# Kernel optimization log

Measured on AMD Instinct MI355X. Metric: run time of the kernel, lower is better.

The kernel has to match this reference:

```python
import jax, jax.numpy as jnp
import numpy as np

NH, NP, MA, FL = 8, 4, 2, 3   # heads, points, max_num_agent, feature_level
L = MA * FL                    # total sampling levels = 6
C = 256
BS, NQ = 8, 4096
SS = np.array([[64, 64], [32, 32], [16, 16]] * MA, dtype=np.int64)  # [L,2] (H,W)
NV = int((SS[:, 0] * SS[:, 1]).sum())  # 10752


def setup_inputs() -> dict:
    key = jax.random.key(0)
    ks = jax.random.split(key, 8)
    f32 = jnp.float32
    return {
        'query': jax.random.normal(ks[0], (BS, NQ, C), f32),
        'query_pos': jax.random.normal(ks[1], (BS, NQ, C), f32),
        'value': jax.random.normal(ks[2], (BS, NV, C), f32),
        'reference_points': jax.random.uniform(ks[3], (BS, NQ, L, 2), f32),
        'spatial_shapes': SS,
        'W_off': jax.random.normal(ks[4], (C, L * NH * NP * 2), f32) * 0.01,
        'b_off': jnp.zeros((L * NH * NP * 2,), f32),
        'W_attn': jax.random.normal(ks[5], (C, L * NH * NP), f32) * 0.05,
        'b_attn': jnp.zeros((L * NH * NP,), f32),
        'W_val': jax.random.normal(ks[6], (C, C), f32) * 0.05,
        'b_val': jnp.zeros((C,), f32),
        'W_out': jax.random.normal(ks[7], (C, C), f32) * 0.05,
        'b_out': jnp.zeros((C,), f32),
    }


def _ms_deform_attn(v, loc, attn, ss):
    # v: [bs, nv, NH, d]; loc: [bs, nq, NH, L, NP, 2] in [0,1] (x,y)
    # attn: [bs, nq, NH, L, NP]; ss: np int array [L,2] (H,W) -- static
    bs, nq = loc.shape[0], loc.shape[1]
    d = v.shape[-1]
    starts = np.concatenate([[0], np.cumsum(ss[:, 0] * ss[:, 1])[:-1]])
    out = jnp.zeros((bs, NH, nq, d), v.dtype)
    for l in range(L):
        H, W = int(ss[l, 0]), int(ss[l, 1])
        s0 = int(starts[l])
        vl = v[:, s0:s0 + H * W].transpose(0, 2, 1, 3)  # [bs, NH, HW, d]
        # sampling coords, grid_sample align_corners=False convention
        x = loc[:, :, :, l, :, 0].transpose(0, 2, 1, 3) * W - 0.5  # [bs,NH,nq,NP]
        y = loc[:, :, :, l, :, 1].transpose(0, 2, 1, 3) * H - 0.5
        x0 = jnp.floor(x); y0 = jnp.floor(y)
        lx = x - x0; ly = y - y0
        x0i = x0.astype(jnp.int32); y0i = y0.astype(jnp.int32)

        def gather(yi, xi):
            valid = (yi >= 0) & (yi < H) & (xi >= 0) & (xi < W)
            idx = jnp.clip(yi, 0, H - 1) * W + jnp.clip(xi, 0, W - 1)  # [bs,NH,nq,NP]
            g = jnp.take_along_axis(vl, idx.reshape(bs, NH, nq * NP, 1), axis=2)
            g = g.reshape(bs, NH, nq, NP, d)
            return g * valid[..., None].astype(g.dtype)  # zero padding outside

        sampled = ((1 - lx) * (1 - ly))[..., None] * gather(y0i, x0i) \
                + (lx * (1 - ly))[..., None] * gather(y0i, x0i + 1) \
                + ((1 - lx) * ly)[..., None] * gather(y0i + 1, x0i) \
                + (lx * ly)[..., None] * gather(y0i + 1, x0i + 1)
        aw = attn[:, :, :, l, :].transpose(0, 2, 1, 3)  # [bs,NH,nq,NP]
        out = out + jnp.einsum('bhqpd,bhqp->bhqd', sampled, aw)
    return out.transpose(0, 2, 1, 3).reshape(bs, nq, NH * d)


def reference(query, query_pos, value, reference_points, spatial_shapes,
              W_off, b_off, W_attn, b_attn, W_val, b_val, W_out, b_out):
    ss = np.asarray(spatial_shapes)
    identity = query
    q = query + query_pos
    bs, nv, c = value.shape
    nq = q.shape[1]
    v = (value @ W_val + b_val).reshape(bs, nv, NH, c // NH)
    off = (q @ W_off + b_off).reshape(bs, nq, NH, L, NP, 2)
    attn = (q @ W_attn + b_attn).reshape(bs, nq, NH, L * NP)
    attn = jax.nn.softmax(attn, axis=-1).reshape(bs, nq, NH, L, NP)
    offset_normalizer = jnp.asarray(np.stack([ss[:, 1], ss[:, 0]], -1), q.dtype)  # [L,2] (W,H)
    loc = reference_points[:, :, None, :, None, :] \
        + off / offset_normalizer[None, None, None, :, None, :]
    out = _ms_deform_attn(v, loc, attn, ss)
    out = out @ W_out + b_out
    return out + identity  # dropout is identity in eval mode
```

## Files before the change

### kernel.cpp

```cpp
#include <hip/hip_runtime.h>

#define NHEAD 8
#define NPOINT 4
#define NLVL 6
#define CDIM 256
#define BSZ 8
#define NQRY 4096
#define NVAL 10752

typedef __attribute__((ext_vector_type(8))) short short8;
typedef __attribute__((ext_vector_type(4))) float floatx4;
typedef __attribute__((ext_vector_type(2))) float float2v;

__device__ __forceinline__ unsigned short f2bf(float f) {
    unsigned u = __float_as_uint(f);
    return (unsigned short)((u + 0x7FFFu + ((u >> 16) & 1u)) >> 16);
}
__device__ __forceinline__ unsigned pack2(float a, float b) {
    return (unsigned)f2bf(a) | ((unsigned)f2bf(b) << 16);
}
__device__ __forceinline__ float blo(unsigned u) { return __uint_as_float(u << 16); }
__device__ __forceinline__ float bhi(unsigned u) { return __uint_as_float(u & 0xffff0000u); }

__device__ __forceinline__ void gload16(const void* g, void* l) {
    __builtin_amdgcn_global_load_lds(
        (const __attribute__((address_space(1))) unsigned int*)g,
        (__attribute__((address_space(3))) unsigned int*)l, 16, 0, 0);
}

__global__ __launch_bounds__(256) void prep_w(
    const float* __restrict__ Wv, const float* __restrict__ Woff,
    const float* __restrict__ Wattn, const float* __restrict__ Wo,
    unsigned short* __restrict__ Wt)
{
    const int id = blockIdx.x * 256 + threadIdx.x;
    const int n = id >> 8, k = id & 255;
    float val;
    if (n < 256) val = Wv[k * 256 + n];
    else if (n < 832) {
        const int nn = n - 256;
        val = (nn < 384) ? Woff[k * 384 + nn] : Wattn[k * 192 + (nn - 384)];
    } else val = Wo[k * 256 + (n - 832)];
    Wt[id] = f2bf(val);
}

__global__ __launch_bounds__(256) void q_conv(
    const float* __restrict__ query, const float* __restrict__ qpos,
    unsigned short* __restrict__ qbf)
{
    const long i = ((long)blockIdx.x * 256 + threadIdx.x) * 4;
    const float4 a = *(const float4*)(query + i);
    const float4 b = *(const float4*)(qpos + i);
    ushort4 r;
    r.x = f2bf(a.x + b.x); r.y = f2bf(a.y + b.y);
    r.z = f2bf(a.z + b.z); r.w = f2bf(a.w + b.w);
    *(ushort4*)(qbf + i) = r;
}

template<int BN, int ABF, int VTRANS, int RESID, int SPLITB>
__global__ __launch_bounds__(512) void gemm_mfma(
    const void* __restrict__ Av, const unsigned short* __restrict__ Bt,
    const float* __restrict__ bias, const float* __restrict__ bias2,
    const float* __restrict__ resid, void* __restrict__ Cv,
    int M, int Ntot)
{
    constexpr int BK = 64, BMt = 128;
    constexpr int WN = BN / 4, NT = WN / 16;
    constexpr int ACH = BMt * (BK / 8);
    constexpr int BCH = BN * (BK / 8);
    constexpr int NCH = ACH + BCH;
    __shared__ char smem[NCH * 16];
    const int tid = threadIdx.x;
    const int bm = blockIdx.y * BMt;
    const int bcol = blockIdx.x * BN;
    const int wid = tid >> 6, lane = tid & 63;
    const int wm = (wid >> 2) * 64, wn = (wid & 3) * WN;
    const int lm = lane & 15;

    floatx4 acc[4][NT];
#pragma unroll
    for (int i = 0; i < 4; ++i)
#pragma unroll
        for (int j = 0; j < NT; ++j) acc[i][j] = (floatx4)0.0f;

    for (int k0 = 0; k0 < 256; k0 += BK) {
        if (ABF) {
            const unsigned short* A = (const unsigned short*)Av;
            constexpr int NI = NCH / 512;
#pragma unroll
            for (int j = 0; j < NI; ++j) {
                const int cbase = (wid * NI + j) * 64;
                const int g = cbase + lane;
                const unsigned short* src;
                if (cbase < ACH) {
                    const int row = g >> 3, c = (g & 7) ^ (row & 7);
                    src = A + (long)(bm + row) * 256 + k0 + c * 8;
                } else {
                    const int g2 = g - ACH;
                    const int row = g2 >> 3, c = (g2 & 7) ^ (row & 7);
                    src = Bt + (long)(bcol + row) * 256 + k0 + c * 8;
                }
                gload16(src, smem + cbase * 16);
            }
        } else {
            constexpr int NIB = BCH / 512;
#pragma unroll
            for (int j = 0; j < NIB; ++j) {
                const int cbase = (wid * NIB + j) * 64;
                const int g2 = cbase + lane;
                const int row = g2 >> 3, c = (g2 & 7) ^ (row & 7);
                gload16(Bt + (long)(bcol + row) * 256 + k0 + c * 8,
                        smem + ACH * 16 + cbase * 16);
            }
            const float* A = (const float*)Av;
#pragma unroll
            for (int j = 0; j < 2; ++j) {
                const int g = j * 512 + tid;
                const int row = g >> 3, c = g & 7;
                const float* p = A + (long)(bm + row) * 256 + k0 + c * 8;
                const float4 a = *(const float4*)p;
                const float4 b = *(const float4*)(p + 4);
                uint4 v;
                v.x = pack2(a.x, a.y); v.y = pack2(a.z, a.w);
                v.z = pack2(b.x, b.y); v.w = pack2(b.z, b.w);
                *(uint4*)(smem + row * 128 + ((c ^ (row & 7)) << 4)) = v;
            }
        }
        __syncthreads();

#pragma unroll
        for (int kk = 0; kk < 2; ++kk) {
            const int cc = kk * 4 + (lane >> 4);
            short8 af[4], bfr[NT];
#pragma unroll
            for (int i = 0; i < 4; ++i) {
                const int row = wm + i * 16 + lm;
                af[i] = *(const short8*)(smem + row * 128 + ((cc ^ (row & 7)) << 4));
            }
#pragma unroll
            for (int j = 0; j < NT; ++j) {
                const int row = wn + j * 16 + lm;
                bfr[j] = *(const short8*)(smem + ACH * 16 + row * 128 + ((cc ^ (row & 7)) << 4));
            }
#pragma unroll
            for (int i = 0; i < 4; ++i)
#pragma unroll
                for (int j = 0; j < NT; ++j)
                    acc[i][j] = __builtin_amdgcn_mfma_f32_16x16x32_bf16(bfr[j], af[i], acc[i][j], 0, 0, 0);
        }
        __syncthreads();
    }

    const int qrow = (lane >> 4) * 4;
#pragma unroll
    for (int j = 0; j < NT; ++j) {
        const int colg = bcol + wn + j * 16 + qrow;
        float4 bv4;
        if (SPLITB && colg >= 384) bv4 = *(const float4*)(bias2 + colg - 384);
        else                       bv4 = *(const float4*)(bias + colg);
#pragma unroll
        for (int i = 0; i < 4; ++i) {
            const int rowl = wm + i * 16 + lm;
            const int rowg = bm + rowl;
            float v0 = acc[i][j][0] + bv4.x;
            float v1 = acc[i][j][1] + bv4.y;
            float v2 = acc[i][j][2] + bv4.z;
            float v3 = acc[i][j][3] + bv4.w;
            if (VTRANS) {
                const int b = bm / NVAL;
                const int pos = bm - b * NVAL + rowl;
                const int h = colg >> 5, d = colg & 31;
                ushort4 o;
                o.x = f2bf(v0); o.y = f2bf(v1); o.z = f2bf(v2); o.w = f2bf(v3);
                *(ushort4*)&((unsigned short*)Cv)[
                    (((long)(b * NHEAD + h)) * NVAL + pos) * 32 + d] = o;
            } else {
                if (RESID) {
                    const float4 rr = *(const float4*)(resid + (long)rowg * 256 + colg);
                    v0 += rr.x; v1 += rr.y; v2 += rr.z; v3 += rr.w;
                }
                float4 o; o.x = v0; o.y = v1; o.z = v2; o.w = v3;
                *(float4*)&((float*)Cv)[(long)rowg * Ntot + colg] = o;
            }
        }
    }
}

__global__ __launch_bounds__(256) void ms_sample4(
    const unsigned short* __restrict__ v,
    const float* __restrict__ oa,
    const float* __restrict__ refp,
    unsigned short* __restrict__ outi)
{
    __shared__ float s_rec[4][192 * 6];
    __shared__ float s_ref[4][12];
    const int tid = threadIdx.x;
    const int w = tid >> 6;
    const int lane = tid & 63;
    const int bq = blockIdx.x * 4 + w;
    const int b = bq >> 12;

    if (lane < 12) s_ref[w][lane] = refp[(long)bq * 12 + lane];
    __syncthreads();

    const int h = lane >> 3;
    const int li = lane & 7;
    const float* oarow = oa + (long)bq * 576;

    const float* lgp = oarow + 384 + h * 24 + li * 3;
    const float lg0 = lgp[0], lg1 = lgp[1], lg2 = lgp[2];
    float mx = fmaxf(lg0, fmaxf(lg1, lg2));
    mx = fmaxf(mx, __shfl_xor(mx, 1));
    mx = fmaxf(mx, __shfl_xor(mx, 2));
    mx = fmaxf(mx, __shfl_xor(mx, 4));
    const float e0 = __expf(lg0 - mx);
    const float e1 = __expf(lg1 - mx);
    const float e2 = __expf(lg2 - mx);
    float den = e0 + e1 + e2;
    den += __shfl_xor(den, 1);
    den += __shfl_xor(den, 2);
    den += __shfl_xor(den, 4);
    const float inv = 1.0f / den;
    const float aw_[3] = {e0 * inv, e1 * inv, e2 * inv};

    const float* offp = oarow + (h * 24 + li * 3) * 2;
    const float2v od0 = *(const float2v*)(offp);
    const float2v od1 = *(const float2v*)(offp + 2);
    const float2v od2 = *(const float2v*)(offp + 4);

#pragma unroll
    for (int k = 0; k < 3; ++k) {
        const int lp = li * 3 + k;
        const int l = lp >> 2;
        const int sh = (l >= 3) ? (l - 3) : l;
        const int W = 64 >> sh;
        const int base = ((l >= 3) ? 5376 : 0)
                       + ((sh >= 1) ? 4096 : 0)
                       + ((sh >= 2) ? 1024 : 0);
        const float Wf = (float)W;
        const float ox = (k == 0) ? od0.x : (k == 1) ? od1.x : od2.x;
        const float oy = (k == 0) ? od0.y : (k == 1) ? od1.y : od2.y;
        const float rx = s_ref[w][l * 2 + 0];
        const float ry = s_ref[w][l * 2 + 1];
        const float x = rx * Wf + ox - 0.5f;
        const float y = ry * Wf + oy - 0.5f;
        const float xf = floorf(x), yf = floorf(y);
        const int x0 = (int)xf, y0 = (int)yf;
        const float lx = x - xf, ly = y - yf;
        const float wx0 = (x0 >= 0 && x0 < W)      ? (1.f - lx) : 0.f;
        const float wx1 = (x0 >= -1 && x0 < W - 1) ? lx         : 0.f;
        const float wy0 = (y0 >= 0 && y0 < W)      ? (1.f - ly) : 0.f;
        const float wy1 = (y0 >= -1 && y0 < W - 1) ? ly         : 0.f;
        const int y0c = min(max(y0, 0), W - 1);
        const int y1c = min(max(y0 + 1, 0), W - 1);
        const int xb = min(max(x0, 0), W - 2);
        const float wl = (xb == x0) ? wx0 : ((xb == x0 + 1) ? wx1 : 0.f);
        const float wr = (xb == x0) ? wx1 : ((xb == x0 - 1) ? wx0 : 0.f);
        const float aw = aw_[k];
        const float awl = aw * wl, awr = aw * wr;
        float* r = &s_rec[w][((lp << 3) + h) * 6];
        float2v wlv, wrv;
        wlv.x = awl * wy0; wlv.y = awl * wy1;
        wrv.x = awr * wy0; wrv.y = awr * wy1;
        *(float2v*)(r)     = wlv;
        *(float2v*)(r + 2) = wrv;
        uint2 pk;
        pk.x = (unsigned)(base + y0c * W + xb) * 64u;
        pk.y = (unsigned)(base + y1c * W + xb) * 64u;
        *(uint2*)(r + 4) = pk;
    }
    __syncthreads();

    const unsigned lane_base =
        (unsigned)((b * NHEAD + h) * NVAL) * 64u + (unsigned)li * 16u;
    const char* vbase = (const char*)v;
    const int sel = (li >> 2) * 2;
    const float* rp0 = &s_rec[w][h * 6];
    float2v a01 = {0.f, 0.f}, a23 = {0.f, 0.f};
    float2v a45 = {0.f, 0.f}, a67 = {0.f, 0.f};

#pragma unroll 8
    for (int lp = 0; lp < NLVL * NPOINT; ++lp) {
        const float* rp = rp0 + lp * 48;
        const float2v wv = *(const float2v*)(rp + sel);
        const uint2 off = *(const uint2*)(rp + 4);
        const uint4 u0 = *(const uint4*)(vbase + (lane_base + off.x));
        const uint4 u1 = *(const uint4*)(vbase + (lane_base + off.y));
        float2v c;
        c.x = blo(u0.x); c.y = bhi(u0.x); a01 += wv.x * c;
        c.x = blo(u0.y); c.y = bhi(u0.y); a23 += wv.x * c;
        c.x = blo(u0.z); c.y = bhi(u0.z); a45 += wv.x * c;
        c.x = blo(u0.w); c.y = bhi(u0.w); a67 += wv.x * c;
        c.x = blo(u1.x); c.y = bhi(u1.x); a01 += wv.y * c;
        c.x = blo(u1.y); c.y = bhi(u1.y); a23 += wv.y * c;
        c.x = blo(u1.z); c.y = bhi(u1.z); a45 += wv.y * c;
        c.x = blo(u1.w); c.y = bhi(u1.w); a67 += wv.y * c;
    }

    a01.x += __shfl_xor(a01.x, 4); a01.y += __shfl_xor(a01.y, 4);
    a23.x += __shfl_xor(a23.x, 4); a23.y += __shfl_xor(a23.y, 4);
    a45.x += __shfl_xor(a45.x, 4); a45.y += __shfl_xor(a45.y, 4);
    a67.x += __shfl_xor(a67.x, 4); a67.y += __shfl_xor(a67.y, 4);

    const int hi = li >> 2;
    const float o0 = hi ? a45.x : a01.x;
    const float o1 = hi ? a45.y : a01.y;
    const float o2 = hi ? a67.x : a23.x;
    const float o3 = hi ? a67.y : a23.y;
    ushort4 o;
    o.x = f2bf(o0); o.y = f2bf(o1); o.z = f2bf(o2); o.w = f2bf(o3);
    const int d = (li & 3) * 8 + hi * 4;
    *(ushort4*)(outi + (long)bq * CDIM + h * 32 + d) = o;
}

extern "C" void kernel_launch(void* const* d_in, const int* in_sizes, int n_in,
                              void* d_out, int out_size, void* d_ws, size_t ws_size,
                              hipStream_t stream) {
    const float* query     = (const float*)d_in[0];
    const float* query_pos = (const float*)d_in[1];
    const float* value     = (const float*)d_in[2];
    const float* refp      = (const float*)d_in[3];
    const float* W_off  = (const float*)d_in[5];
    const float* b_off  = (const float*)d_in[6];
    const float* W_attn = (const float*)d_in[7];
    const float* b_attn = (const float*)d_in[8];
    const float* W_val  = (const float*)d_in[9];
    const float* b_val  = (const float*)d_in[10];
    const float* W_out  = (const float*)d_in[11];
    const float* b_out  = (const float*)d_in[12];
    float* out = (float*)d_out;

    unsigned short* v_bf = (unsigned short*)d_ws;
    unsigned short* q_bf = v_bf + (long)86016 * 256;
    unsigned short* Wt   = q_bf + (long)32768 * 256;
    float* oa_ws = (float*)(Wt + (long)1088 * 256);
    unsigned short* i_bf = (unsigned short*)(oa_ws + (long)32768 * 576);

    const int MV = BSZ * NVAL;
    const int MQ = BSZ * NQRY;

    prep_w<<<1088, 256, 0, stream>>>(W_val, W_off, W_attn, W_out, Wt);
    q_conv<<<(MQ * CDIM / 4) / 256, 256, 0, stream>>>(query, query_pos, q_bf);
    gemm_mfma<256, 0, 1, 0, 0><<<dim3(1, MV / 128), 512, 0, stream>>>(
        value, Wt, b_val, nullptr, nullptr, v_bf, MV, 256);
    gemm_mfma<192, 1, 0, 0, 1><<<dim3(3, MQ / 128), 512, 0, stream>>>(
        q_bf, Wt + (long)256 * 256, b_off, b_attn, nullptr, oa_ws, MQ, 576);
    ms_sample4<<<MQ / 4, 256, 0, stream>>>(v_bf, oa_ws, refp, i_bf);
    gemm_mfma<256, 1, 0, 1, 0><<<dim3(1, MQ / 128), 512, 0, stream>>>(
        i_bf, Wt + (long)832 * 256, b_out, nullptr, query, out, MQ, 256);
}
```

Baseline: 367.7 us.

## Fuse query+pos add into offset GEMM, narrow GEMM tiles, interleave sampler batches

Removes the separate q_conv kernel by having the offset/attention GEMM read query and query_pos in fp32, add them, and convert to bf16 while staging A tiles. The value and output GEMMs switch from BN=256 with one column block to BN=128 with two column blocks, doubling grid size for more parallelism at the cost of reloading A tiles twice. The sampler kernel now maps consecutive blocks to different batches, spreading concurrent gathers across batch value slices. In exchange, the fused GEMM reads twice the fp32 A traffic per column block, three times over.

```diff
diff --git a/kernel.cpp b/kernel.cpp
--- a/kernel.cpp
+++ b/kernel.cpp
@@ -44,22 +44,10 @@
     Wt[id] = f2bf(val);
 }
 
-__global__ __launch_bounds__(256) void q_conv(
-    const float* __restrict__ query, const float* __restrict__ qpos,
-    unsigned short* __restrict__ qbf)
-{
-    const long i = ((long)blockIdx.x * 256 + threadIdx.x) * 4;
-    const float4 a = *(const float4*)(query + i);
-    const float4 b = *(const float4*)(qpos + i);
-    ushort4 r;
-    r.x = f2bf(a.x + b.x); r.y = f2bf(a.y + b.y);
-    r.z = f2bf(a.z + b.z); r.w = f2bf(a.w + b.w);
-    *(ushort4*)(qbf + i) = r;
-}
-
-template<int BN, int ABF, int VTRANS, int RESID, int SPLITB>
+template<int BN, int AMODE, int VTRANS, int RESID, int SPLITB>
 __global__ __launch_bounds__(512) void gemm_mfma(
-    const void* __restrict__ Av, const unsigned short* __restrict__ Bt,
+    const void* __restrict__ Av, const float* __restrict__ A2,
+    const unsigned short* __restrict__ Bt,
     const float* __restrict__ bias, const float* __restrict__ bias2,
     const float* __restrict__ resid, void* __restrict__ Cv,
     int M, int Ntot)
@@ -84,7 +72,7 @@
         for (int j = 0; j < NT; ++j) acc[i][j] = (floatx4)0.0f;
 
     for (int k0 = 0; k0 < 256; k0 += BK) {
-        if (ABF) {
+        if (AMODE == 1) {
             const unsigned short* A = (const unsigned short*)Av;
             constexpr int NI = NCH / 512;
 #pragma unroll
@@ -117,9 +105,15 @@
             for (int j = 0; j < 2; ++j) {
                 const int g = j * 512 + tid;
                 const int row = g >> 3, c = g & 7;
-                const float* p = A + (long)(bm + row) * 256 + k0 + c * 8;
-                const float4 a = *(const float4*)p;
-                const float4 b = *(const float4*)(p + 4);
+                const long off = (long)(bm + row) * 256 + k0 + c * 8;
+                float4 a = *(const float4*)(A + off);
+                float4 b = *(const float4*)(A + off + 4);
+                if (AMODE == 2) {
+                    const float4 a2 = *(const float4*)(A2 + off);
+                    const float4 b2 = *(const float4*)(A2 + off + 4);
+                    a.x += a2.x; a.y += a2.y; a.z += a2.z; a.w += a2.w;
+                    b.x += b2.x; b.y += b2.y; b.z += b2.z; b.w += b2.w;
+                }
                 uint4 v;
                 v.x = pack2(a.x, a.y); v.y = pack2(a.z, a.w);
                 v.z = pack2(b.x, b.y); v.w = pack2(b.z, b.w);
@@ -197,8 +191,8 @@
     const int tid = threadIdx.x;
     const int w = tid >> 6;
     const int lane = tid & 63;
-    const int bq = blockIdx.x * 4 + w;
-    const int b = bq >> 12;
+    const int b = blockIdx.x & 7;
+    const int bq = b * NQRY + (blockIdx.x >> 3) * 4 + w;
 
     if (lane < 12) s_ref[w][lane] = refp[(long)bq * 12 + lane];
     __syncthreads();
@@ -340,12 +334,11 @@
     const int MQ = BSZ * NQRY;
 
     prep_w<<<1088, 256, 0, stream>>>(W_val, W_off, W_attn, W_out, Wt);
-    q_conv<<<(MQ * CDIM / 4) / 256, 256, 0, stream>>>(query, query_pos, q_bf);
-    gemm_mfma<256, 0, 1, 0, 0><<<dim3(1, MV / 128), 512, 0, stream>>>(
-        value, Wt, b_val, nullptr, nullptr, v_bf, MV, 256);
-    gemm_mfma<192, 1, 0, 0, 1><<<dim3(3, MQ / 128), 512, 0, stream>>>(
-        q_bf, Wt + (long)256 * 256, b_off, b_attn, nullptr, oa_ws, MQ, 576);
+    gemm_mfma<128, 0, 1, 0, 0><<<dim3(2, MV / 128), 512, 0, stream>>>(
+        value, nullptr, Wt, b_val, nullptr, nullptr, v_bf, MV, 256);
+    gemm_mfma<192, 2, 0, 0, 1><<<dim3(3, MQ / 128), 512, 0, stream>>>(
+        query, query_pos, Wt + (long)256 * 256, b_off, b_attn, nullptr, oa_ws, MQ, 576);
     ms_sample4<<<MQ / 4, 256, 0, stream>>>(v_bf, oa_ws, refp, i_bf);
-    gemm_mfma<256, 1, 0, 1, 0><<<dim3(1, MQ / 128), 512, 0, stream>>>(
-        i_bf, Wt + (long)832 * 256, b_out, nullptr, query, out, MQ, 256);
-}
+    gemm_mfma<128, 1, 0, 1, 0><<<dim3(2, MQ / 128), 512, 0, stream>>>(
+        i_bf, nullptr, Wt + (long)832 * 256, b_out, nullptr, query, out, MQ, 256);
+}
```

After: 373.7 us. Within noise of the previous version (+1.6%).

## Double-buffer GEMM shared-memory tiles and prefetch next K-slice during MFMA

Applied to the files above, without the earlier changes.

The GEMM K loop now keeps two shared-memory stages and issues the global loads for the next 64-wide K slice before the current slice's MFMAs run. For fp32 A inputs, the loads go to registers and are converted to bf16 and written to the other buffer after compute. This hides global-load latency behind matrix math and removes one barrier per iteration. In exchange it doubles LDS use and adds register pressure, which may lower occupancy.

```diff
diff --git a/kernel.cpp b/kernel.cpp
--- a/kernel.cpp
+++ b/kernel.cpp
@@ -57,7 +57,7 @@
     *(ushort4*)(qbf + i) = r;
 }
 
-template<int BN, int ABF, int VTRANS, int RESID, int SPLITB>
+template<int BN, int AMODE, int VTRANS, int RESID, int SPLITB>
 __global__ __launch_bounds__(512) void gemm_mfma(
     const void* __restrict__ Av, const unsigned short* __restrict__ Bt,
     const float* __restrict__ bias, const float* __restrict__ bias2,
@@ -69,7 +69,7 @@
     constexpr int ACH = BMt * (BK / 8);
     constexpr int BCH = BN * (BK / 8);
     constexpr int NCH = ACH + BCH;
-    __shared__ char smem[NCH * 16];
+    __shared__ char smem[2][NCH * 16];
     const int tid = threadIdx.x;
     const int bm = blockIdx.y * BMt;
     const int bcol = blockIdx.x * BN;
@@ -83,8 +83,31 @@
 #pragma unroll
         for (int j = 0; j < NT; ++j) acc[i][j] = (floatx4)0.0f;
 
-    for (int k0 = 0; k0 < 256; k0 += BK) {
-        if (ABF) {
+    float4 ra[2][2];
+
+    auto ALOAD = [&](int k0) {
+#pragma unroll
+        for (int j = 0; j < 2; ++j) {
+            const int g = j * 512 + tid;
+            const int row = g >> 3, c = g & 7;
+            const float* p = (const float*)Av + (long)(bm + row) * 256 + k0 + c * 8;
+            ra[j][0] = *(const float4*)p;
+            ra[j][1] = *(const float4*)(p + 4);
+        }
+    };
+    auto AWRITE = [&](char* sm) {
+#pragma unroll
+        for (int j = 0; j < 2; ++j) {
+            const int g = j * 512 + tid;
+            const int row = g >> 3, c = g & 7;
+            uint4 v;
+            v.x = pack2(ra[j][0].x, ra[j][0].y); v.y = pack2(ra[j][0].z, ra[j][0].w);
+            v.z = pack2(ra[j][1].x, ra[j][1].y); v.w = pack2(ra[j][1].z, ra[j][1].w);
+            *(uint4*)(sm + row * 128 + ((c ^ (row & 7)) << 4)) = v;
+        }
+    };
+    auto BSTAGE = [&](int k0, char* sm) {
+        if (AMODE == 1) {
             const unsigned short* A = (const unsigned short*)Av;
             constexpr int NI = NCH / 512;
 #pragma unroll
@@ -100,7 +123,7 @@
                     const int row = g2 >> 3, c = (g2 & 7) ^ (row & 7);
                     src = Bt + (long)(bcol + row) * 256 + k0 + c * 8;
                 }
-                gload16(src, smem + cbase * 16);
+                gload16(src, sm + cbase * 16);
             }
         } else {
             constexpr int NIB = BCH / 512;
@@ -110,24 +133,24 @@
                 const int g2 = cbase + lane;
                 const int row = g2 >> 3, c = (g2 & 7) ^ (row & 7);
                 gload16(Bt + (long)(bcol + row) * 256 + k0 + c * 8,
-                        smem + ACH * 16 + cbase * 16);
-            }
-            const float* A = (const float*)Av;
-#pragma unroll
-            for (int j = 0; j < 2; ++j) {
-                const int g = j * 512 + tid;
-                const int row = g >> 3, c = g & 7;
-                const float* p = A + (long)(bm + row) * 256 + k0 + c * 8;
-                const float4 a = *(const float4*)p;
-                const float4 b = *(const float4*)(p + 4);
-                uint4 v;
-                v.x = pack2(a.x, a.y); v.y = pack2(a.z, a.w);
-                v.z = pack2(b.x, b.y); v.w = pack2(b.z, b.w);
-                *(uint4*)(smem + row * 128 + ((c ^ (row & 7)) << 4)) = v;
-            }
-        }
-        __syncthreads();
-
+                        sm + ACH * 16 + cbase * 16);
+            }
+        }
+    };
+
+    if (AMODE == 0) ALOAD(0);
+    BSTAGE(0, smem[0]);
+    if (AMODE == 0) AWRITE(smem[0]);
+    __syncthreads();
+
+    int cur = 0;
+    for (int t = 0; t < 4; ++t) {
+        if (t < 3) {
+            if (AMODE == 0) ALOAD((t + 1) * BK);
+            BSTAGE((t + 1) * BK, smem[cur ^ 1]);
+        }
+        char* sA = smem[cur];
+        char* sB = smem[cur] + ACH * 16;
 #pragma unroll
         for (int kk = 0; kk < 2; ++kk) {
             const int cc = kk * 4 + (lane >> 4);
@@ -135,12 +158,12 @@
 #pragma unroll
             for (int i = 0; i < 4; ++i) {
                 const int row = wm + i * 16 + lm;
-                af[i] = *(const short8*)(smem + row * 128 + ((cc ^ (row & 7)) << 4));
+                af[i] = *(const short8*)(sA + row * 128 + ((cc ^ (row & 7)) << 4));
             }
 #pragma unroll
             for (int j = 0; j < NT; ++j) {
                 const int row = wn + j * 16 + lm;
-                bfr[j] = *(const short8*)(smem + ACH * 16 + row * 128 + ((cc ^ (row & 7)) << 4));
+                bfr[j] = *(const short8*)(sB + row * 128 + ((cc ^ (row & 7)) << 4));
             }
 #pragma unroll
             for (int i = 0; i < 4; ++i)
@@ -148,7 +171,9 @@
                 for (int j = 0; j < NT; ++j)
                     acc[i][j] = __builtin_amdgcn_mfma_f32_16x16x32_bf16(bfr[j], af[i], acc[i][j], 0, 0, 0);
         }
+        if (t < 3 && AMODE == 0) AWRITE(smem[cur ^ 1]);
         __syncthreads();
+        cur ^= 1;
     }
 
     const int qrow = (lane >> 4) * 4;
```

Result: slower. 383.6 us (+4.3%).

## Merge value and query GEMMs into one launch, narrow output GEMM tiles

Applied to the files above, without the earlier changes.

The value projection GEMM and the offset/attention projection GEMM are turned into a shared device body and launched together as one grid of 1440 blocks. Blocks are interleaved 7:8 between the two problems so both run concurrently and fill the GPU better. The final output GEMM switches from 256-wide to 128-wide column tiles, which doubles its block count for better occupancy. In exchange, blocks reserve the larger shared-memory footprint, and tile loads for the B matrix repeat more often in the output GEMM.

```diff
diff --git a/kernel.cpp b/kernel.cpp
--- a/kernel.cpp
+++ b/kernel.cpp
@@ -57,22 +57,19 @@
     *(ushort4*)(qbf + i) = r;
 }
 
-template<int BN, int ABF, int VTRANS, int RESID, int SPLITB>
-__global__ __launch_bounds__(512) void gemm_mfma(
+template<int BN, int AMODE, int VTRANS, int RESID, int SPLITB>
+__device__ __forceinline__ void gemm_body(
     const void* __restrict__ Av, const unsigned short* __restrict__ Bt,
     const float* __restrict__ bias, const float* __restrict__ bias2,
     const float* __restrict__ resid, void* __restrict__ Cv,
-    int M, int Ntot)
+    int bm, int bcol, char* smem, int Ntot)
 {
     constexpr int BK = 64, BMt = 128;
     constexpr int WN = BN / 4, NT = WN / 16;
     constexpr int ACH = BMt * (BK / 8);
     constexpr int BCH = BN * (BK / 8);
     constexpr int NCH = ACH + BCH;
-    __shared__ char smem[NCH * 16];
     const int tid = threadIdx.x;
-    const int bm = blockIdx.y * BMt;
-    const int bcol = blockIdx.x * BN;
     const int wid = tid >> 6, lane = tid & 63;
     const int wm = (wid >> 2) * 64, wn = (wid & 3) * WN;
     const int lm = lane & 15;
@@ -84,7 +81,7 @@
         for (int j = 0; j < NT; ++j) acc[i][j] = (floatx4)0.0f;
 
     for (int k0 = 0; k0 < 256; k0 += BK) {
-        if (ABF) {
+        if (AMODE == 1) {
             const unsigned short* A = (const unsigned short*)Av;
             constexpr int NI = NCH / 512;
 #pragma unroll
@@ -184,6 +181,38 @@
             }
         }
     }
+}
+
+__global__ __launch_bounds__(512) void gemm_fused(
+    const float* __restrict__ value, const unsigned short* __restrict__ qbf,
+    const unsigned short* __restrict__ Wt,
+    const float* __restrict__ b_val, const float* __restrict__ b_off,
+    const float* __restrict__ b_attn,
+    unsigned short* __restrict__ v_bf, float* __restrict__ oa)
+{
+    __shared__ char smem[49152];
+    const int id = blockIdx.x;
+    const int grp = id / 15, r = id % 15;
+    if (r < 7) {
+        const int t = grp * 7 + r;
+        gemm_body<256, 0, 1, 0, 0>(value, Wt, b_val, nullptr, nullptr,
+                                   v_bf, t * 128, 0, smem, 256);
+    } else {
+        const int t = grp * 8 + (r - 7);
+        gemm_body<192, 1, 0, 0, 1>(qbf, Wt + (long)256 * 256, b_off, b_attn,
+                                   nullptr, oa, (t / 3) * 128, (t % 3) * 192,
+                                   smem, 576);
+    }
+}
+
+__global__ __launch_bounds__(512) void gemm3_k(
+    const unsigned short* __restrict__ ibf, const unsigned short* __restrict__ Wt,
+    const float* __restrict__ b_out, const float* __restrict__ query,
+    float* __restrict__ out)
+{
+    __shared__ char smem[32768];
+    gemm_body<128, 1, 0, 1, 0>(ibf, Wt, b_out, nullptr, query, out,
+                               blockIdx.y * 128, blockIdx.x * 128, smem, 256);
 }
 
 __global__ __launch_bounds__(256) void ms_sample4(
@@ -336,16 +365,13 @@
     float* oa_ws = (float*)(Wt + (long)1088 * 256);
     unsigned short* i_bf = (unsigned short*)(oa_ws + (long)32768 * 576);
 
-    const int MV = BSZ * NVAL;
     const int MQ = BSZ * NQRY;
 
     prep_w<<<1088, 256, 0, stream>>>(W_val, W_off, W_attn, W_out, Wt);
     q_conv<<<(MQ * CDIM / 4) / 256, 256, 0, stream>>>(query, query_pos, q_bf);
-    gemm_mfma<256, 0, 1, 0, 0><<<dim3(1, MV / 128), 512, 0, stream>>>(
-        value, Wt, b_val, nullptr, nullptr, v_bf, MV, 256);
-    gemm_mfma<192, 1, 0, 0, 1><<<dim3(3, MQ / 128), 512, 0, stream>>>(
-        q_bf, Wt + (long)256 * 256, b_off, b_attn, nullptr, oa_ws, MQ, 576);
+    gemm_fused<<<1440, 512, 0, stream>>>(
+        value, q_bf, Wt, b_val, b_off, b_attn, v_bf, oa_ws);
     ms_sample4<<<MQ / 4, 256, 0, stream>>>(v_bf, oa_ws, refp, i_bf);
-    gemm_mfma<256, 1, 0, 1, 0><<<dim3(1, MQ / 128), 512, 0, stream>>>(
-        i_bf, Wt + (long)832 * 256, b_out, nullptr, query, out, MQ, 256);
-}
+    gemm3_k<<<dim3(2, MQ / 128), 512, 0, stream>>>(
+        i_bf, Wt + (long)832 * 256, b_out, query, out);
+}
```

Result: no change. 363.1 us (-1.3%).
